# Optimization experiments

Measured on AMD Instinct MI355X. Metric: run time of the kernel, lower is better.

The kernel has to match this reference:

```python
import jax, jax.numpy as jnp
import numpy as np

NUM_NODES = 50000
FEAT_DIM = 64
HIDDEN = 128
OUT_DIM = 128
NUM_EDGES = 640000


def setup_inputs() -> dict:
    key = jax.random.key(0)
    ks = jax.random.split(key, 8)
    edge_index = jax.random.randint(ks[0], (2, NUM_EDGES), 0, NUM_NODES, dtype=jnp.int32)
    emb = jax.random.normal(ks[1], (NUM_NODES, FEAT_DIM), dtype=jnp.float32) * 0.1
    # SAGEConv: lin_l (aggregated neighbors, with bias) and lin_r (root, no bias)
    s1 = 1.0 / np.sqrt(FEAT_DIM)
    W1l = jax.random.uniform(ks[2], (HIDDEN, FEAT_DIM), jnp.float32, -s1, s1)
    b1l = jnp.zeros((HIDDEN,), jnp.float32)
    W1r = jax.random.uniform(ks[3], (HIDDEN, FEAT_DIM), jnp.float32, -s1, s1)
    s2 = 1.0 / np.sqrt(HIDDEN)
    W2l = jax.random.uniform(ks[4], (OUT_DIM, HIDDEN), jnp.float32, -s2, s2)
    b2l = jnp.zeros((OUT_DIM,), jnp.float32)
    W2r = jax.random.uniform(ks[5], (OUT_DIM, HIDDEN), jnp.float32, -s2, s2)
    return {"edge_index": edge_index, "emb": emb, "W1l": W1l, "b1l": b1l,
            "W1r": W1r, "W2l": W2l, "b2l": b2l, "W2r": W2r}


def _sage_conv(x, src, dst, Wl, bl, Wr):
    # mean-aggregate source features at target nodes, then two linear paths
    msg = x[src]                                   # [E, d]
    agg = jax.ops.segment_sum(msg, dst, num_segments=NUM_NODES)
    deg = jax.ops.segment_sum(jnp.ones((src.shape[0],), x.dtype), dst,
                              num_segments=NUM_NODES)
    mean = agg / jnp.maximum(deg, 1.0)[:, None]    # [N, d]
    return mean @ Wl.T + bl + x @ Wr.T             # [N, out]


def reference(edge_index, emb, W1l, b1l, W1r, W2l, b2l, W2r):
    src, dst = edge_index[0], edge_index[1]
    h = jax.nn.relu(_sage_conv(emb, src, dst, W1l, b1l, W1r))
    return _sage_conv(h, src, dst, W2l, b2l, W2r)
```

## Files before the change

### kernel.cpp

```cpp
#include <hip/hip_runtime.h>

#define N_NODES 50000
#define FEAT    64
#define HID     128
#define N_EDGES 640000
#define NBLK    196
#define GCAP    64

typedef __attribute__((ext_vector_type(8))) short bf16x8;
typedef __attribute__((ext_vector_type(4))) float f32x4;

static __device__ __forceinline__ unsigned short f2bf(float f) {
    unsigned u = __float_as_uint(f);
    u = u + 0x7fffu + ((u >> 16) & 1u);
    return (unsigned short)(u >> 16);
}

static __device__ __forceinline__ void gridbar(int* bar, int gen) {
    __syncthreads();
    if (threadIdx.x == 0) {
        __threadfence();
        int arrived = atomicAdd(&bar[0], 1);
        if (arrived == NBLK - 1) {
            atomicExch(&bar[0], 0);
            __threadfence();
            atomicExch(&bar[1], gen);
        } else {
            while (atomicAdd(&bar[1], 0) < gen) __builtin_amdgcn_s_sleep(2);
        }
        __threadfence();
    }
    __syncthreads();
}

__global__ __launch_bounds__(256) void histcvt_kernel(
        const int* __restrict__ dst, const float* __restrict__ emb,
        const float* __restrict__ W1l, const float* __restrict__ W1r,
        const float* __restrict__ W2l, const float* __restrict__ W2r,
        int* __restrict__ count,
        unsigned* __restrict__ emb_bf_u, unsigned* __restrict__ Wbf_u) {
    int gtid = blockIdx.x * 256 + threadIdx.x;
    if (gtid < N_EDGES) atomicAdd(&count[dst[gtid]], 1);
    for (int i = gtid; i < N_NODES * FEAT / 2; i += N_EDGES) {
        float2 v = ((const float2*)emb)[i];
        emb_bf_u[i] = ((unsigned)f2bf(v.y) << 16) | (unsigned)f2bf(v.x);
    }
    if (gtid < 24576) {
        int w = gtid * 2;
        float lo, hi;
        if (w < 8192)       { lo = W1l[w];         hi = W1l[w + 1]; }
        else if (w < 16384) { lo = W1r[w - 8192];  hi = W1r[w - 8191]; }
        else if (w < 32768) { lo = W2l[w - 16384]; hi = W2l[w - 16383]; }
        else                { lo = W2r[w - 32768]; hi = W2r[w - 32767]; }
        Wbf_u[gtid] = ((unsigned)f2bf(hi) << 16) | (unsigned)f2bf(lo);
    }
}

__global__ __launch_bounds__(256) void scanperm_kernel(
        const int* __restrict__ count, int* offset, int* dhist, int* dcur,
        int* bsum, int* boff, int* dstart, int* perm, int* bar) {
    __shared__ int tmp[256];
    __shared__ int lh[64];
    __shared__ int lb2[64];
    int t = threadIdx.x;
    int gtid = blockIdx.x * 256 + t;

    {
        if (t < 64) lh[t] = 0;
        int v = (gtid < N_NODES) ? count[gtid] : 0;
        tmp[t] = v;
        __syncthreads();
        if (gtid < N_NODES) atomicAdd(&lh[v < 63 ? v : 63], 1);
        for (int off = 1; off < 256; off <<= 1) {
            int add = (t >= off) ? tmp[t - off] : 0;
            __syncthreads();
            tmp[t] += add;
            __syncthreads();
        }
        if (gtid < N_NODES) offset[gtid] = tmp[t] - v;
        if (t == 255) bsum[blockIdx.x] = tmp[255];
        if (t < 64 && lh[t] > 0) atomicAdd(&dhist[t], lh[t]);
    }
    gridbar(bar, 1);

    if (blockIdx.x < 2) {
        const int* in  = (blockIdx.x == 0) ? bsum : dhist;
        int*       out = (blockIdx.x == 0) ? boff : dstart;
        int cnt        = (blockIdx.x == 0) ? NBLK : 64;
        int v = (t < cnt) ? in[t] : 0;
        tmp[t] = v;
        __syncthreads();
        for (int off = 1; off < 256; off <<= 1) {
            int add = (t >= off) ? tmp[t - off] : 0;
            __syncthreads();
            tmp[t] += add;
            __syncthreads();
        }
        if (t < cnt) out[t] = tmp[t] - v;
    }
    gridbar(bar, 2);

    if (gtid < N_NODES) offset[gtid] += boff[blockIdx.x];
    if (gtid == 0) offset[N_NODES] = N_EDGES;
    {
        if (t < 64) lh[t] = 0;
        __syncthreads();
        int d = 0, slot = 0;
        if (gtid < N_NODES) {
            int c = count[gtid];
            d = c < 63 ? c : 63;
            slot = atomicAdd(&lh[d], 1);
        }
        __syncthreads();
        if (t < 64 && lh[t] > 0) lb2[t] = atomicAdd(&dcur[t], lh[t]);
        __syncthreads();
        if (gtid < N_NODES) perm[dstart[d] + lb2[d] + slot] = gtid;
    }
}

__global__ void fill_kernel(const int* __restrict__ src, const int* __restrict__ dst,
                            const int* __restrict__ offset, int* __restrict__ cursor,
                            int* __restrict__ esrc) {
    int e = blockIdx.x * blockDim.x + threadIdx.x;
    if (e >= N_EDGES) return;
    int d = dst[e];
    int slot = atomicAdd(&cursor[d], 1);
    esrc[offset[d] + slot] = src[e];
}

__global__ __launch_bounds__(256) void gather1_kernel(
        const float4* __restrict__ emb4, const int* __restrict__ offset,
        const int* __restrict__ esrc, const int* __restrict__ perm,
        uint4* __restrict__ mean1_u4) {
    __shared__ int sidx[4][8][GCAP];
    int t = threadIdx.x, wave = t >> 6, lane = t & 63;
    int sub = lane >> 3, fl = lane & 7;
    int widx = blockIdx.x * 32 + wave * 8 + sub;
    bool valid = widx < N_NODES;
    int n = 0, beg = 0, deg = 0;
    if (valid) { n = perm[widx]; beg = offset[n]; deg = offset[n + 1] - beg; }
    bool fast = deg <= GCAP;
    if (valid && fast) {
        for (int j = fl; j < deg; j += 8) sidx[wave][sub][j] = esrc[beg + j];
    }
    __syncthreads();
    float a[8] = {0.f,0.f,0.f,0.f,0.f,0.f,0.f,0.f};
    if (valid) {
        #define ACC1(v) { \
            unsigned ux=__float_as_uint((v).x),uy=__float_as_uint((v).y); \
            unsigned uz=__float_as_uint((v).z),uw=__float_as_uint((v).w); \
            a[0]+=__uint_as_float(ux<<16); a[1]+=__uint_as_float(ux&0xffff0000u); \
            a[2]+=__uint_as_float(uy<<16); a[3]+=__uint_as_float(uy&0xffff0000u); \
            a[4]+=__uint_as_float(uz<<16); a[5]+=__uint_as_float(uz&0xffff0000u); \
            a[6]+=__uint_as_float(uw<<16); a[7]+=__uint_as_float(uw&0xffff0000u); }
        if (fast) {
            int i = 0;
            for (; i + 8 <= deg; i += 8) {
                float4 v0 = emb4[sidx[wave][sub][i+0]*8+fl];
                float4 v1 = emb4[sidx[wave][sub][i+1]*8+fl];
                float4 v2 = emb4[sidx[wave][sub][i+2]*8+fl];
                float4 v3 = emb4[sidx[wave][sub][i+3]*8+fl];
                float4 v4 = emb4[sidx[wave][sub][i+4]*8+fl];
                float4 v5 = emb4[sidx[wave][sub][i+5]*8+fl];
                float4 v6 = emb4[sidx[wave][sub][i+6]*8+fl];
                float4 v7 = emb4[sidx[wave][sub][i+7]*8+fl];
                ACC1(v0) ACC1(v1) ACC1(v2) ACC1(v3)
                ACC1(v4) ACC1(v5) ACC1(v6) ACC1(v7)
            }
            for (; i + 4 <= deg; i += 4) {
                float4 v0 = emb4[sidx[wave][sub][i+0]*8+fl];
                float4 v1 = emb4[sidx[wave][sub][i+1]*8+fl];
                float4 v2 = emb4[sidx[wave][sub][i+2]*8+fl];
                float4 v3 = emb4[sidx[wave][sub][i+3]*8+fl];
                ACC1(v0) ACC1(v1) ACC1(v2) ACC1(v3)
            }
            for (; i < deg; ++i) { float4 v = emb4[sidx[wave][sub][i]*8+fl]; ACC1(v) }
        } else {
            for (int i = 0; i < deg; ++i) { float4 v = emb4[esrc[beg+i]*8+fl]; ACC1(v) }
        }
        float dinv = 1.0f / fmaxf((float)deg, 1.0f);
        uint4 o;
        o.x = ((unsigned)f2bf(a[1]*dinv) << 16) | (unsigned)f2bf(a[0]*dinv);
        o.y = ((unsigned)f2bf(a[3]*dinv) << 16) | (unsigned)f2bf(a[2]*dinv);
        o.z = ((unsigned)f2bf(a[5]*dinv) << 16) | (unsigned)f2bf(a[4]*dinv);
        o.w = ((unsigned)f2bf(a[7]*dinv) << 16) | (unsigned)f2bf(a[6]*dinv);
        mean1_u4[n*8 + fl] = o;
    }
}

__global__ __launch_bounds__(256) void gather2_kernel(
        const float4* __restrict__ h4, const int* __restrict__ offset,
        const int* __restrict__ esrc, const int* __restrict__ perm,
        uint4* __restrict__ mean2_u4) {
    __shared__ int sidx[4][4][GCAP];
    int t = threadIdx.x, wave = t >> 6, lane = t & 63;
    int sub = lane >> 4, fl = lane & 15;
    int widx = blockIdx.x * 16 + wave * 4 + sub;
    bool valid = widx < N_NODES;
    int n = 0, beg = 0, deg = 0;
    if (valid) { n = perm[widx]; beg = offset[n]; deg = offset[n + 1] - beg; }
    bool fast = deg <= GCAP;
    if (valid && fast) {
        for (int j = fl; j < deg; j += 16) sidx[wave][sub][j] = esrc[beg + j];
    }
    __syncthreads();
    float a[8] = {0.f,0.f,0.f,0.f,0.f,0.f,0.f,0.f};
    if (valid) {
        if (fast) {
            int i = 0;
            for (; i + 8 <= deg; i += 8) {
                float4 v0 = h4[sidx[wave][sub][i+0]*16+fl];
                float4 v1 = h4[sidx[wave][sub][i+1]*16+fl];
                float4 v2 = h4[sidx[wave][sub][i+2]*16+fl];
                float4 v3 = h4[sidx[wave][sub][i+3]*16+fl];
                float4 v4 = h4[sidx[wave][sub][i+4]*16+fl];
                float4 v5 = h4[sidx[wave][sub][i+5]*16+fl];
                float4 v6 = h4[sidx[wave][sub][i+6]*16+fl];
                float4 v7 = h4[sidx[wave][sub][i+7]*16+fl];
                ACC1(v0) ACC1(v1) ACC1(v2) ACC1(v3)
                ACC1(v4) ACC1(v5) ACC1(v6) ACC1(v7)
            }
            for (; i + 4 <= deg; i += 4) {
                float4 v0 = h4[sidx[wave][sub][i+0]*16+fl];
                float4 v1 = h4[sidx[wave][sub][i+1]*16+fl];
                float4 v2 = h4[sidx[wave][sub][i+2]*16+fl];
                float4 v3 = h4[sidx[wave][sub][i+3]*16+fl];
                ACC1(v0) ACC1(v1) ACC1(v2) ACC1(v3)
            }
            for (; i < deg; ++i) { float4 v = h4[sidx[wave][sub][i]*16+fl]; ACC1(v) }
        } else {
            for (int i = 0; i < deg; ++i) { float4 v = h4[esrc[beg+i]*16+fl]; ACC1(v) }
        }
        float dinv = 1.0f / fmaxf((float)deg, 1.0f);
        uint4 o;
        o.x = ((unsigned)f2bf(a[1]*dinv) << 16) | (unsigned)f2bf(a[0]*dinv);
        o.y = ((unsigned)f2bf(a[3]*dinv) << 16) | (unsigned)f2bf(a[2]*dinv);
        o.z = ((unsigned)f2bf(a[5]*dinv) << 16) | (unsigned)f2bf(a[4]*dinv);
        o.w = ((unsigned)f2bf(a[7]*dinv) << 16) | (unsigned)f2bf(a[6]*dinv);
        mean2_u4[n*16 + fl] = o;
    }
}

__global__ __launch_bounds__(256) void gemm1_kernel(
        const short* __restrict__ mean1, const short* __restrict__ embb,
        const short* __restrict__ Wl, const short* __restrict__ Wr,
        const float* __restrict__ bias, unsigned short* __restrict__ hout) {
    int wid = blockIdx.x * 4 + (threadIdx.x >> 6);
    if (wid >= N_NODES / 16) return;
    int lane = threadIdx.x & 63;
    int col = lane & 15, quad = lane >> 4;
    int m0 = wid * 16;
    f32x4 acc[8];
    #pragma unroll
    for (int nt = 0; nt < 8; ++nt) acc[nt] = (f32x4){0.f,0.f,0.f,0.f};
    #pragma unroll
    for (int kb = 0; kb < FEAT; kb += 32) {
        bf16x8 a = *(const bf16x8*)(mean1 + (m0 + col) * FEAT + kb + quad * 8);
        #pragma unroll
        for (int nt = 0; nt < 8; ++nt) {
            bf16x8 b = *(const bf16x8*)(Wl + (nt * 16 + col) * FEAT + kb + quad * 8);
            acc[nt] = __builtin_amdgcn_mfma_f32_16x16x32_bf16(a, b, acc[nt], 0, 0, 0);
        }
    }
    #pragma unroll
    for (int kb = 0; kb < FEAT; kb += 32) {
        bf16x8 a = *(const bf16x8*)(embb + (m0 + col) * FEAT + kb + quad * 8);
        #pragma unroll
        for (int nt = 0; nt < 8; ++nt) {
            bf16x8 b = *(const bf16x8*)(Wr + (nt * 16 + col) * FEAT + kb + quad * 8);
            acc[nt] = __builtin_amdgcn_mfma_f32_16x16x32_bf16(a, b, acc[nt], 0, 0, 0);
        }
    }
    #pragma unroll
    for (int nt = 0; nt < 8; ++nt) {
        float bv = bias[nt * 16 + col];
        #pragma unroll
        for (int r = 0; r < 4; ++r) {
            float v = fmaxf(acc[nt][r] + bv, 0.f);
            hout[(m0 + quad * 4 + r) * HID + nt * 16 + col] = f2bf(v);
        }
    }
}

__global__ __launch_bounds__(256) void gemm2_kernel(
        const short* __restrict__ mean2, const short* __restrict__ hbf,
        const short* __restrict__ Wl, const short* __restrict__ Wr,
        const float* __restrict__ bias, float* __restrict__ out) {
    int wid = blockIdx.x * 4 + (threadIdx.x >> 6);
    if (wid >= N_NODES / 16) return;
    int lane = threadIdx.x & 63;
    int col = lane & 15, quad = lane >> 4;
    int m0 = wid * 16;
    f32x4 acc[8];
    #pragma unroll
    for (int nt = 0; nt < 8; ++nt) acc[nt] = (f32x4){0.f,0.f,0.f,0.f};
    #pragma unroll
    for (int kb = 0; kb < HID; kb += 32) {
        bf16x8 a = *(const bf16x8*)(mean2 + (m0 + col) * HID + kb + quad * 8);
        #pragma unroll
        for (int nt = 0; nt < 8; ++nt) {
            bf16x8 b = *(const bf16x8*)(Wl + (nt * 16 + col) * HID + kb + quad * 8);
            acc[nt] = __builtin_amdgcn_mfma_f32_16x16x32_bf16(a, b, acc[nt], 0, 0, 0);
        }
    }
    #pragma unroll
    for (int kb = 0; kb < HID; kb += 32) {
        bf16x8 a = *(const bf16x8*)(hbf + (m0 + col) * HID + kb + quad * 8);
        #pragma unroll
        for (int nt = 0; nt < 8; ++nt) {
            bf16x8 b = *(const bf16x8*)(Wr + (nt * 16 + col) * HID + kb + quad * 8);
            acc[nt] = __builtin_amdgcn_mfma_f32_16x16x32_bf16(a, b, acc[nt], 0, 0, 0);
        }
    }
    #pragma unroll
    for (int nt = 0; nt < 8; ++nt) {
        float bv = bias[nt * 16 + col];
        #pragma unroll
        for (int r = 0; r < 4; ++r) {
            out[(m0 + quad * 4 + r) * HID + nt * 16 + col] = acc[nt][r] + bv;
        }
    }
}

extern "C" void kernel_launch(void* const* d_in, const int* in_sizes, int n_in,
                              void* d_out, int out_size, void* d_ws, size_t ws_size,
                              hipStream_t stream) {
    const int*   edge_index = (const int*)d_in[0];
    const float* emb        = (const float*)d_in[1];
    const float* W1l        = (const float*)d_in[2];
    const float* b1l        = (const float*)d_in[3];
    const float* W1r        = (const float*)d_in[4];
    const float* W2l        = (const float*)d_in[5];
    const float* b2l        = (const float*)d_in[6];
    const float* W2r        = (const float*)d_in[7];
    float* out = (float*)d_out;

    const int* src = edge_index;
    const int* dst = edge_index + N_EDGES;

    int* iws    = (int*)d_ws;
    int* offset = iws;
    int* count  = iws + 50004;
    int* cursor = iws + 100004;
    int* dhist  = iws + 150004;
    int* dcur   = iws + 150068;
    int* bar    = iws + 150132;
    int* bsum   = iws + 150136;
    int* boff   = iws + 150392;
    int* dstart = iws + 150648;
    int* perm   = iws + 150712;
    int* esrc   = iws + 200712;
    unsigned short* W1l_bf = (unsigned short*)(iws + 840712);
    unsigned short* W1r_bf = (unsigned short*)(iws + 844808);
    unsigned short* W2l_bf = (unsigned short*)(iws + 848904);
    unsigned short* W2r_bf = (unsigned short*)(iws + 857096);
    unsigned short* Wbf    = W1l_bf;
    unsigned short* emb_bf = (unsigned short*)(iws + 865288);
    unsigned short* mean1  = (unsigned short*)(iws + 2465288);
    unsigned short* hbf    = (unsigned short*)(iws + 4065288);
    unsigned short* mean2  = (unsigned short*)(iws + 7265288);

    (void)hipMemsetAsync(count, 0, (size_t)(150136 - 50004) * sizeof(int), stream);

    histcvt_kernel<<<(N_EDGES + 255) / 256, 256, 0, stream>>>(
        dst, emb, W1l, W1r, W2l, W2r, count, (unsigned*)emb_bf, (unsigned*)Wbf);
    scanperm_kernel<<<NBLK, 256, 0, stream>>>(
        count, offset, dhist, dcur, bsum, boff, dstart, perm, bar);
    fill_kernel<<<(N_EDGES + 255) / 256, 256, 0, stream>>>(
        src, dst, offset, cursor, esrc);

    gather1_kernel<<<(N_NODES + 31) / 32, 256, 0, stream>>>(
        (const float4*)emb_bf, offset, esrc, perm, (uint4*)mean1);
    gemm1_kernel<<<(N_NODES / 16 + 3) / 4, 256, 0, stream>>>(
        (const short*)mean1, (const short*)emb_bf,
        (const short*)W1l_bf, (const short*)W1r_bf, b1l, hbf);
    gather2_kernel<<<(N_NODES + 15) / 16, 256, 0, stream>>>(
        (const float4*)hbf, offset, esrc, perm, (uint4*)mean2);
    gemm2_kernel<<<(N_NODES / 16 + 3) / 4, 256, 0, stream>>>(
        (const short*)mean2, (const short*)hbf,
        (const short*)W2l_bf, (const short*)W2r_bf, b2l, out);
}
```

Baseline: 271.8 us.

## Fuse neighbor gather-mean into GEMM kernels and reuse histogram atomic slots

```diff
diff --git a/kernel.cpp b/kernel.cpp
--- a/kernel.cpp
+++ b/kernel.cpp
@@ -14,6 +14,12 @@
     unsigned u = __float_as_uint(f);
     u = u + 0x7fffu + ((u >> 16) & 1u);
     return (unsigned short)(u >> 16);
+}
+static __device__ __forceinline__ float bflo(unsigned u) {
+    return __uint_as_float(u << 16);
+}
+static __device__ __forceinline__ float bfhi(unsigned u) {
+    return __uint_as_float(u & 0xffff0000u);
 }
 
 static __device__ __forceinline__ void gridbar(int* bar, int gen) {
@@ -37,10 +43,13 @@
         const int* __restrict__ dst, const float* __restrict__ emb,
         const float* __restrict__ W1l, const float* __restrict__ W1r,
         const float* __restrict__ W2l, const float* __restrict__ W2r,
-        int* __restrict__ count,
+        int* __restrict__ count, int* __restrict__ eslot,
         unsigned* __restrict__ emb_bf_u, unsigned* __restrict__ Wbf_u) {
     int gtid = blockIdx.x * 256 + threadIdx.x;
-    if (gtid < N_EDGES) atomicAdd(&count[dst[gtid]], 1);
+    if (gtid < N_EDGES) {
+        int slot = atomicAdd(&count[dst[gtid]], 1);
+        eslot[gtid] = slot;
+    }
     for (int i = gtid; i < N_NODES * FEAT / 2; i += N_EDGES) {
         float2 v = ((const float2*)emb)[i];
         emb_bf_u[i] = ((unsigned)f2bf(v.y) << 16) | (unsigned)f2bf(v.x);
@@ -119,206 +128,177 @@
 }
 
 __global__ void fill_kernel(const int* __restrict__ src, const int* __restrict__ dst,
-                            const int* __restrict__ offset, int* __restrict__ cursor,
-                            int* __restrict__ esrc) {
+                            const int* __restrict__ offset,
+                            const int* __restrict__ eslot, int* __restrict__ esrc) {
     int e = blockIdx.x * blockDim.x + threadIdx.x;
     if (e >= N_EDGES) return;
-    int d = dst[e];
-    int slot = atomicAdd(&cursor[d], 1);
-    esrc[offset[d] + slot] = src[e];
-}
-
-__global__ __launch_bounds__(256) void gather1_kernel(
-        const float4* __restrict__ emb4, const int* __restrict__ offset,
+    esrc[offset[dst[e]] + eslot[e]] = src[e];
+}
+
+__global__ __launch_bounds__(256) void fgemm1_kernel(
+        const unsigned short* __restrict__ embb, const int* __restrict__ offset,
         const int* __restrict__ esrc, const int* __restrict__ perm,
-        uint4* __restrict__ mean1_u4) {
-    __shared__ int sidx[4][8][GCAP];
-    int t = threadIdx.x, wave = t >> 6, lane = t & 63;
-    int sub = lane >> 3, fl = lane & 7;
-    int widx = blockIdx.x * 32 + wave * 8 + sub;
-    bool valid = widx < N_NODES;
-    int n = 0, beg = 0, deg = 0;
-    if (valid) { n = perm[widx]; beg = offset[n]; deg = offset[n + 1] - beg; }
-    bool fast = deg <= GCAP;
-    if (valid && fast) {
-        for (int j = fl; j < deg; j += 8) sidx[wave][sub][j] = esrc[beg + j];
-    }
-    __syncthreads();
-    float a[8] = {0.f,0.f,0.f,0.f,0.f,0.f,0.f,0.f};
-    if (valid) {
-        #define ACC1(v) { \
-            unsigned ux=__float_as_uint((v).x),uy=__float_as_uint((v).y); \
-            unsigned uz=__float_as_uint((v).z),uw=__float_as_uint((v).w); \
-            a[0]+=__uint_as_float(ux<<16); a[1]+=__uint_as_float(ux&0xffff0000u); \
-            a[2]+=__uint_as_float(uy<<16); a[3]+=__uint_as_float(uy&0xffff0000u); \
-            a[4]+=__uint_as_float(uz<<16); a[5]+=__uint_as_float(uz&0xffff0000u); \
-            a[6]+=__uint_as_float(uw<<16); a[7]+=__uint_as_float(uw&0xffff0000u); }
-        if (fast) {
-            int i = 0;
-            for (; i + 8 <= deg; i += 8) {
-                float4 v0 = emb4[sidx[wave][sub][i+0]*8+fl];
-                float4 v1 = emb4[sidx[wave][sub][i+1]*8+fl];
-                float4 v2 = emb4[sidx[wave][sub][i+2]*8+fl];
-                float4 v3 = emb4[sidx[wave][sub][i+3]*8+fl];
-                float4 v4 = emb4[sidx[wave][sub][i+4]*8+fl];
-                float4 v5 = emb4[sidx[wave][sub][i+5]*8+fl];
-                float4 v6 = emb4[sidx[wave][sub][i+6]*8+fl];
-                float4 v7 = emb4[sidx[wave][sub][i+7]*8+fl];
-                ACC1(v0) ACC1(v1) ACC1(v2) ACC1(v3)
-                ACC1(v4) ACC1(v5) ACC1(v6) ACC1(v7)
-            }
-            for (; i + 4 <= deg; i += 4) {
-                float4 v0 = emb4[sidx[wave][sub][i+0]*8+fl];
-                float4 v1 = emb4[sidx[wave][sub][i+1]*8+fl];
-                float4 v2 = emb4[sidx[wave][sub][i+2]*8+fl];
-                float4 v3 = emb4[sidx[wave][sub][i+3]*8+fl];
-                ACC1(v0) ACC1(v1) ACC1(v2) ACC1(v3)
-            }
-            for (; i < deg; ++i) { float4 v = emb4[sidx[wave][sub][i]*8+fl]; ACC1(v) }
-        } else {
-            for (int i = 0; i < deg; ++i) { float4 v = emb4[esrc[beg+i]*8+fl]; ACC1(v) }
-        }
-        float dinv = 1.0f / fmaxf((float)deg, 1.0f);
-        uint4 o;
-        o.x = ((unsigned)f2bf(a[1]*dinv) << 16) | (unsigned)f2bf(a[0]*dinv);
-        o.y = ((unsigned)f2bf(a[3]*dinv) << 16) | (unsigned)f2bf(a[2]*dinv);
-        o.z = ((unsigned)f2bf(a[5]*dinv) << 16) | (unsigned)f2bf(a[4]*dinv);
-        o.w = ((unsigned)f2bf(a[7]*dinv) << 16) | (unsigned)f2bf(a[6]*dinv);
-        mean1_u4[n*8 + fl] = o;
-    }
-}
-
-__global__ __launch_bounds__(256) void gather2_kernel(
-        const float4* __restrict__ h4, const int* __restrict__ offset,
-        const int* __restrict__ esrc, const int* __restrict__ perm,
-        uint4* __restrict__ mean2_u4) {
-    __shared__ int sidx[4][4][GCAP];
-    int t = threadIdx.x, wave = t >> 6, lane = t & 63;
-    int sub = lane >> 4, fl = lane & 15;
-    int widx = blockIdx.x * 16 + wave * 4 + sub;
-    bool valid = widx < N_NODES;
-    int n = 0, beg = 0, deg = 0;
-    if (valid) { n = perm[widx]; beg = offset[n]; deg = offset[n + 1] - beg; }
-    bool fast = deg <= GCAP;
-    if (valid && fast) {
-        for (int j = fl; j < deg; j += 16) sidx[wave][sub][j] = esrc[beg + j];
-    }
-    __syncthreads();
-    float a[8] = {0.f,0.f,0.f,0.f,0.f,0.f,0.f,0.f};
-    if (valid) {
-        if (fast) {
-            int i = 0;
-            for (; i + 8 <= deg; i += 8) {
-                float4 v0 = h4[sidx[wave][sub][i+0]*16+fl];
-                float4 v1 = h4[sidx[wave][sub][i+1]*16+fl];
-                float4 v2 = h4[sidx[wave][sub][i+2]*16+fl];
-                float4 v3 = h4[sidx[wave][sub][i+3]*16+fl];
-                float4 v4 = h4[sidx[wave][sub][i+4]*16+fl];
-                float4 v5 = h4[sidx[wave][sub][i+5]*16+fl];
-                float4 v6 = h4[sidx[wave][sub][i+6]*16+fl];
-                float4 v7 = h4[sidx[wave][sub][i+7]*16+fl];
-                ACC1(v0) ACC1(v1) ACC1(v2) ACC1(v3)
-                ACC1(v4) ACC1(v5) ACC1(v6) ACC1(v7)
-            }
-            for (; i + 4 <= deg; i += 4) {
-                float4 v0 = h4[sidx[wave][sub][i+0]*16+fl];
-                float4 v1 = h4[sidx[wave][sub][i+1]*16+fl];
-                float4 v2 = h4[sidx[wave][sub][i+2]*16+fl];
-                float4 v3 = h4[sidx[wave][sub][i+3]*16+fl];
-                ACC1(v0) ACC1(v1) ACC1(v2) ACC1(v3)
-            }
-            for (; i < deg; ++i) { float4 v = h4[sidx[wave][sub][i]*16+fl]; ACC1(v) }
-        } else {
-            for (int i = 0; i < deg; ++i) { float4 v = h4[esrc[beg+i]*16+fl]; ACC1(v) }
-        }
-        float dinv = 1.0f / fmaxf((float)deg, 1.0f);
-        uint4 o;
-        o.x = ((unsigned)f2bf(a[1]*dinv) << 16) | (unsigned)f2bf(a[0]*dinv);
-        o.y = ((unsigned)f2bf(a[3]*dinv) << 16) | (unsigned)f2bf(a[2]*dinv);
-        o.z = ((unsigned)f2bf(a[5]*dinv) << 16) | (unsigned)f2bf(a[4]*dinv);
-        o.w = ((unsigned)f2bf(a[7]*dinv) << 16) | (unsigned)f2bf(a[6]*dinv);
-        mean2_u4[n*16 + fl] = o;
-    }
-}
-
-__global__ __launch_bounds__(256) void gemm1_kernel(
-        const short* __restrict__ mean1, const short* __restrict__ embb,
         const short* __restrict__ Wl, const short* __restrict__ Wr,
         const float* __restrict__ bias, unsigned short* __restrict__ hout) {
-    int wid = blockIdx.x * 4 + (threadIdx.x >> 6);
-    if (wid >= N_NODES / 16) return;
-    int lane = threadIdx.x & 63;
+    __shared__ unsigned short smean[16][72];
+    __shared__ int sidx[16][GCAP];
+    __shared__ int nid[16];
+    int t = threadIdx.x;
+    if (t < 16) nid[t] = perm[blockIdx.x * 16 + t];
+    __syncthreads();
+
+    int sub = t >> 4, fl = t & 15;
+    int n = nid[sub];
+    int beg = offset[n], deg = offset[n + 1] - beg;
+    bool fast = deg <= GCAP;
+    if (fast) { for (int j = fl; j < deg; j += 16) sidx[sub][j] = esrc[beg + j]; }
+    float A0[4] = {0,0,0,0}, A1[4] = {0,0,0,0}, A2[4] = {0,0,0,0}, A3[4] = {0,0,0,0};
+    const uint2* eb2 = (const uint2*)embb;
+    {
+        int i = 0;
+        if (fast) {
+            for (; i + 4 <= deg; i += 4) {
+                uint2 v0 = eb2[(size_t)sidx[sub][i+0] * 16 + fl];
+                uint2 v1 = eb2[(size_t)sidx[sub][i+1] * 16 + fl];
+                uint2 v2 = eb2[(size_t)sidx[sub][i+2] * 16 + fl];
+                uint2 v3 = eb2[(size_t)sidx[sub][i+3] * 16 + fl];
+                A0[0]+=bflo(v0.x); A0[1]+=bfhi(v0.x); A0[2]+=bflo(v0.y); A0[3]+=bfhi(v0.y);
+                A1[0]+=bflo(v1.x); A1[1]+=bfhi(v1.x); A1[2]+=bflo(v1.y); A1[3]+=bfhi(v1.y);
+                A2[0]+=bflo(v2.x); A2[1]+=bfhi(v2.x); A2[2]+=bflo(v2.y); A2[3]+=bfhi(v2.y);
+                A3[0]+=bflo(v3.x); A3[1]+=bfhi(v3.x); A3[2]+=bflo(v3.y); A3[3]+=bfhi(v3.y);
+            }
+            for (; i < deg; ++i) {
+                uint2 v = eb2[(size_t)sidx[sub][i] * 16 + fl];
+                A0[0]+=bflo(v.x); A0[1]+=bfhi(v.x); A0[2]+=bflo(v.y); A0[3]+=bfhi(v.y);
+            }
+        } else {
+            for (; i < deg; ++i) {
+                uint2 v = eb2[(size_t)esrc[beg + i] * 16 + fl];
+                A0[0]+=bflo(v.x); A0[1]+=bfhi(v.x); A0[2]+=bflo(v.y); A0[3]+=bfhi(v.y);
+            }
+        }
+    }
+    float dinv = 1.0f / fmaxf((float)deg, 1.0f);
+    float s0 = ((A0[0]+A1[0])+(A2[0]+A3[0])) * dinv;
+    float s1 = ((A0[1]+A1[1])+(A2[1]+A3[1])) * dinv;
+    float s2 = ((A0[2]+A1[2])+(A2[2]+A3[2])) * dinv;
+    float s3 = ((A0[3]+A1[3])+(A2[3]+A3[3])) * dinv;
+    uint2 o;
+    o.x = ((unsigned)f2bf(s1) << 16) | (unsigned)f2bf(s0);
+    o.y = ((unsigned)f2bf(s3) << 16) | (unsigned)f2bf(s2);
+    *(uint2*)&smean[sub][fl * 4] = o;
+    __syncthreads();
+
+    int wave = t >> 6, lane = t & 63;
     int col = lane & 15, quad = lane >> 4;
-    int m0 = wid * 16;
-    f32x4 acc[8];
-    #pragma unroll
-    for (int nt = 0; nt < 8; ++nt) acc[nt] = (f32x4){0.f,0.f,0.f,0.f};
+    int ncol = nid[col];
+    int nt0 = wave * 2, nt1 = nt0 + 1;
+    f32x4 acc0 = (f32x4){0.f,0.f,0.f,0.f}, acc1 = (f32x4){0.f,0.f,0.f,0.f};
     #pragma unroll
     for (int kb = 0; kb < FEAT; kb += 32) {
-        bf16x8 a = *(const bf16x8*)(mean1 + (m0 + col) * FEAT + kb + quad * 8);
-        #pragma unroll
-        for (int nt = 0; nt < 8; ++nt) {
-            bf16x8 b = *(const bf16x8*)(Wl + (nt * 16 + col) * FEAT + kb + quad * 8);
-            acc[nt] = __builtin_amdgcn_mfma_f32_16x16x32_bf16(a, b, acc[nt], 0, 0, 0);
-        }
-    }
-    #pragma unroll
-    for (int kb = 0; kb < FEAT; kb += 32) {
-        bf16x8 a = *(const bf16x8*)(embb + (m0 + col) * FEAT + kb + quad * 8);
-        #pragma unroll
-        for (int nt = 0; nt < 8; ++nt) {
-            bf16x8 b = *(const bf16x8*)(Wr + (nt * 16 + col) * FEAT + kb + quad * 8);
-            acc[nt] = __builtin_amdgcn_mfma_f32_16x16x32_bf16(a, b, acc[nt], 0, 0, 0);
-        }
-    }
-    #pragma unroll
-    for (int nt = 0; nt < 8; ++nt) {
-        float bv = bias[nt * 16 + col];
-        #pragma unroll
-        for (int r = 0; r < 4; ++r) {
-            float v = fmaxf(acc[nt][r] + bv, 0.f);
-            hout[(m0 + quad * 4 + r) * HID + nt * 16 + col] = f2bf(v);
-        }
-    }
-}
-
-__global__ __launch_bounds__(256) void gemm2_kernel(
-        const short* __restrict__ mean2, const short* __restrict__ hbf,
+        bf16x8 am = *(const bf16x8*)&smean[col][kb + quad * 8];
+        bf16x8 ax = *(const bf16x8*)(embb + (size_t)ncol * FEAT + kb + quad * 8);
+        bf16x8 bl0 = *(const bf16x8*)(Wl + (nt0 * 16 + col) * FEAT + kb + quad * 8);
+        bf16x8 br0 = *(const bf16x8*)(Wr + (nt0 * 16 + col) * FEAT + kb + quad * 8);
+        bf16x8 bl1 = *(const bf16x8*)(Wl + (nt1 * 16 + col) * FEAT + kb + quad * 8);
+        bf16x8 br1 = *(const bf16x8*)(Wr + (nt1 * 16 + col) * FEAT + kb + quad * 8);
+        acc0 = __builtin_amdgcn_mfma_f32_16x16x32_bf16(am, bl0, acc0, 0, 0, 0);
+        acc0 = __builtin_amdgcn_mfma_f32_16x16x32_bf16(ax, br0, acc0, 0, 0, 0);
+        acc1 = __builtin_amdgcn_mfma_f32_16x16x32_bf16(am, bl1, acc1, 0, 0, 0);
+        acc1 = __builtin_amdgcn_mfma_f32_16x16x32_bf16(ax, br1, acc1, 0, 0, 0);
+    }
+    float bv0 = bias[nt0 * 16 + col];
+    float bv1 = bias[nt1 * 16 + col];
+    #pragma unroll
+    for (int r = 0; r < 4; ++r) {
+        int node = nid[quad * 4 + r];
+        hout[(size_t)node * HID + nt0 * 16 + col] = f2bf(fmaxf(acc0[r] + bv0, 0.f));
+        hout[(size_t)node * HID + nt1 * 16 + col] = f2bf(fmaxf(acc1[r] + bv1, 0.f));
+    }
+}
+
+__global__ __launch_bounds__(256) void fgemm2_kernel(
+        const unsigned short* __restrict__ hbf, const int* __restrict__ offset,
+        const int* __restrict__ esrc, const int* __restrict__ perm,
         const short* __restrict__ Wl, const short* __restrict__ Wr,
         const float* __restrict__ bias, float* __restrict__ out) {
-    int wid = blockIdx.x * 4 + (threadIdx.x >> 6);
-    if (wid >= N_NODES / 16) return;
-    int lane = threadIdx.x & 63;
+    __shared__ unsigned short smean[16][136];
+    __shared__ int sidx[16][GCAP];
+    __shared__ int nid[16];
+    int t = threadIdx.x;
+    if (t < 16) nid[t] = perm[blockIdx.x * 16 + t];
+    __syncthreads();
+
+    int sub = t >> 4, fl = t & 15;
+    int n = nid[sub];
+    int beg = offset[n], deg = offset[n + 1] - beg;
+    bool fast = deg <= GCAP;
+    if (fast) { for (int j = fl; j < deg; j += 16) sidx[sub][j] = esrc[beg + j]; }
+    float A0[8] = {0,0,0,0,0,0,0,0}, A1[8] = {0,0,0,0,0,0,0,0};
+    float A2[8] = {0,0,0,0,0,0,0,0}, A3[8] = {0,0,0,0,0,0,0,0};
+    const uint4* hb4 = (const uint4*)hbf;
+    #define ACCU(A, v) { \
+        A[0]+=bflo((v).x); A[1]+=bfhi((v).x); A[2]+=bflo((v).y); A[3]+=bfhi((v).y); \
+        A[4]+=bflo((v).z); A[5]+=bfhi((v).z); A[6]+=bflo((v).w); A[7]+=bfhi((v).w); }
+    {
+        int i = 0;
+        if (fast) {
+            for (; i + 4 <= deg; i += 4) {
+                uint4 v0 = hb4[(size_t)sidx[sub][i+0] * 16 + fl];
+                uint4 v1 = hb4[(size_t)sidx[sub][i+1] * 16 + fl];
+                uint4 v2 = hb4[(size_t)sidx[sub][i+2] * 16 + fl];
+                uint4 v3 = hb4[(size_t)sidx[sub][i+3] * 16 + fl];
+                ACCU(A0, v0) ACCU(A1, v1) ACCU(A2, v2) ACCU(A3, v3)
+            }
+            for (; i < deg; ++i) {
+                uint4 v = hb4[(size_t)sidx[sub][i] * 16 + fl];
+                ACCU(A0, v)
+            }
+        } else {
+            for (; i < deg; ++i) {
+                uint4 v = hb4[(size_t)esrc[beg + i] * 16 + fl];
+                ACCU(A0, v)
+            }
+        }
+    }
+    #undef ACCU
+    float dinv = 1.0f / fmaxf((float)deg, 1.0f);
+    unsigned ow[4];
+    #pragma unroll
+    for (int k = 0; k < 4; ++k) {
+        float lo = ((A0[2*k]+A1[2*k])+(A2[2*k]+A3[2*k])) * dinv;
+        float hi = ((A0[2*k+1]+A1[2*k+1])+(A2[2*k+1]+A3[2*k+1])) * dinv;
+        ow[k] = ((unsigned)f2bf(hi) << 16) | (unsigned)f2bf(lo);
+    }
+    uint4 o4 = {ow[0], ow[1], ow[2], ow[3]};
+    *(uint4*)&smean[sub][fl * 8] = o4;
+    __syncthreads();
+
+    int wave = t >> 6, lane = t & 63;
     int col = lane & 15, quad = lane >> 4;
-    int m0 = wid * 16;
-    f32x4 acc[8];
-    #pragma unroll
-    for (int nt = 0; nt < 8; ++nt) acc[nt] = (f32x4){0.f,0.f,0.f,0.f};
+    int ncol = nid[col];
+    int nt0 = wave * 2, nt1 = nt0 + 1;
+    f32x4 acc0 = (f32x4){0.f,0.f,0.f,0.f}, acc1 = (f32x4){0.f,0.f,0.f,0.f};
     #pragma unroll
     for (int kb = 0; kb < HID; kb += 32) {
-        bf16x8 a = *(const bf16x8*)(mean2 + (m0 + col) * HID + kb + quad * 8);
-        #pragma unroll
-        for (int nt = 0; nt < 8; ++nt) {
-            bf16x8 b = *(const bf16x8*)(Wl + (nt * 16 + col) * HID + kb + quad * 8);
-            acc[nt] = __builtin_amdgcn_mfma_f32_16x16x32_bf16(a, b, acc[nt], 0, 0, 0);
-        }
-    }
-    #pragma unroll
-    for (int kb = 0; kb < HID; kb += 32) {
-        bf16x8 a = *(const bf16x8*)(hbf + (m0 + col) * HID + kb + quad * 8);
-        #pragma unroll
-        for (int nt = 0; nt < 8; ++nt) {
-            bf16x8 b = *(const bf16x8*)(Wr + (nt * 16 + col) * HID + kb + quad * 8);
-            acc[nt] = __builtin_amdgcn_mfma_f32_16x16x32_bf16(a, b, acc[nt], 0, 0, 0);
-        }
-    }
-    #pragma unroll
-    for (int nt = 0; nt < 8; ++nt) {
-        float bv = bias[nt * 16 + col];
-        #pragma unroll
-        for (int r = 0; r < 4; ++r) {
-            out[(m0 + quad * 4 + r) * HID + nt * 16 + col] = acc[nt][r] + bv;
-        }
+        bf16x8 am = *(const bf16x8*)&smean[col][kb + quad * 8];
+        bf16x8 ax = *(const bf16x8*)(hbf + (size_t)ncol * HID + kb + quad * 8);
+        bf16x8 bl0 = *(const bf16x8*)(Wl + (nt0 * 16 + col) * HID + kb + quad * 8);
+        bf16x8 br0 = *(const bf16x8*)(Wr + (nt0 * 16 + col) * HID + kb + quad * 8);
+        bf16x8 bl1 = *(const bf16x8*)(Wl + (nt1 * 16 + col) * HID + kb + quad * 8);
+        bf16x8 br1 = *(const bf16x8*)(Wr + (nt1 * 16 + col) * HID + kb + quad * 8);
+        acc0 = __builtin_amdgcn_mfma_f32_16x16x32_bf16(am, bl0, acc0, 0, 0, 0);
+        acc0 = __builtin_amdgcn_mfma_f32_16x16x32_bf16(ax, br0, acc0, 0, 0, 0);
+        acc1 = __builtin_amdgcn_mfma_f32_16x16x32_bf16(am, bl1, acc1, 0, 0, 0);
+        acc1 = __builtin_amdgcn_mfma_f32_16x16x32_bf16(ax, br1, acc1, 0, 0, 0);
+    }
+    float bv0 = bias[nt0 * 16 + col];
+    float bv1 = bias[nt1 * 16 + col];
+    #pragma unroll
+    for (int r = 0; r < 4; ++r) {
+        int node = nid[quad * 4 + r];
+        out[(size_t)node * HID + nt0 * 16 + col] = acc0[r] + bv0;
+        out[(size_t)node * HID + nt1 * 16 + col] = acc1[r] + bv1;
     }
 }
 
@@ -341,42 +321,37 @@
     int* iws    = (int*)d_ws;
     int* offset = iws;
     int* count  = iws + 50004;
-    int* cursor = iws + 100004;
-    int* dhist  = iws + 150004;
-    int* dcur   = iws + 150068;
-    int* bar    = iws + 150132;
-    int* bsum   = iws + 150136;
-    int* boff   = iws + 150392;
-    int* dstart = iws + 150648;
-    int* perm   = iws + 150712;
-    int* esrc   = iws + 200712;
-    unsigned short* W1l_bf = (unsigned short*)(iws + 840712);
-    unsigned short* W1r_bf = (unsigned short*)(iws + 844808);
-    unsigned short* W2l_bf = (unsigned short*)(iws + 848904);
-    unsigned short* W2r_bf = (unsigned short*)(iws + 857096);
+    int* dhist  = iws + 100004;
+    int* dcur   = iws + 100068;
+    int* bar    = iws + 100132;
+    int* bsum   = iws + 100136;
+    int* boff   = iws + 100392;
+    int* dstart = iws + 100648;
+    int* perm   = iws + 100712;
+    int* esrc   = iws + 150712;
+    int* eslot  = iws + 790712;
+    unsigned short* W1l_bf = (unsigned short*)(iws + 1430712);
+    unsigned short* W1r_bf = (unsigned short*)(iws + 1434808);
+    unsigned short* W2l_bf = (unsigned short*)(iws + 1438904);
+    unsigned short* W2r_bf = (unsigned short*)(iws + 1447096);
     unsigned short* Wbf    = W1l_bf;
-    unsigned short* emb_bf = (unsigned short*)(iws + 865288);
-    unsigned short* mean1  = (unsigned short*)(iws + 2465288);
-    unsigned short* hbf    = (unsigned short*)(iws + 4065288);
-    unsigned short* mean2  = (unsigned short*)(iws + 7265288);
-
-    (void)hipMemsetAsync(count, 0, (size_t)(150136 - 50004) * sizeof(int), stream);
+    unsigned short* emb_bf = (unsigned short*)(iws + 1455288);
+    unsigned short* hbf    = (unsigned short*)(iws + 3055288);
+
+    (void)hipMemsetAsync(count, 0, (size_t)(100136 - 50004) * sizeof(int), stream);
 
     histcvt_kernel<<<(N_EDGES + 255) / 256, 256, 0, stream>>>(
-        dst, emb, W1l, W1r, W2l, W2r, count, (unsigned*)emb_bf, (unsigned*)Wbf);
+        dst, emb, W1l, W1r, W2l, W2r, count, eslot,
+        (unsigned*)emb_bf, (unsigned*)Wbf);
     scanperm_kernel<<<NBLK, 256, 0, stream>>>(
         count, offset, dhist, dcur, bsum, boff, dstart, perm, bar);
     fill_kernel<<<(N_EDGES + 255) / 256, 256, 0, stream>>>(
-        src, dst, offset, cursor, esrc);
-
-    gather1_kernel<<<(N_NODES + 31) / 32, 256, 0, stream>>>(
-        (const float4*)emb_bf, offset, esrc, perm, (uint4*)mean1);
-    gemm1_kernel<<<(N_NODES / 16 + 3) / 4, 256, 0, stream>>>(
-        (const short*)mean1, (const short*)emb_bf,
+        src, dst, offset, eslot, esrc);
+
+    fgemm1_kernel<<<N_NODES / 16, 256, 0, stream>>>(
+        emb_bf, offset, esrc, perm,
         (const short*)W1l_bf, (const short*)W1r_bf, b1l, hbf);
-    gather2_kernel<<<(N_NODES + 15) / 16, 256, 0, stream>>>(
-        (const float4*)hbf, offset, esrc, perm, (uint4*)mean2);
-    gemm2_kernel<<<(N_NODES / 16 + 3) / 4, 256, 0, stream>>>(
-        (const short*)mean2, (const short*)hbf,
+    fgemm2_kernel<<<N_NODES / 16, 256, 0, stream>>>(
+        hbf, offset, esrc, perm,
         (const short*)W2l_bf, (const short*)W2r_bf, b2l, out);
 }
```

Result: faster. 231.7 us (-14.8%).
